# Performance work log

Measured on AMD Instinct MI355X. Metric: run time of the kernel, lower is better.

Reference implementation:

```python
import jax, jax.numpy as jnp
import numpy as np

EPS = 1e-12
H = 256
W = 256
RANK = 4
CTX = 1024
BATCH = 32
FF = (H + W) * RANK * 4  # 8192
STD = 0.001


def _norm(x, axis):
    # torch: (x - mean) / sqrt(var(unbiased) + eps)
    m = jnp.mean(x, axis=axis, keepdims=True)
    v = jnp.var(x, axis=axis, keepdims=True, ddof=1)
    return (x - m) / jnp.sqrt(v + EPS)


def _norm_polar(x):
    # x: [B, N, 2]; magnitude-normalize relative to per-batch max magnitude
    x_abs = jnp.sqrt(x[..., 0] ** 2 + x[..., 1] ** 2 + EPS)          # [B, N]
    h = x_abs / (jnp.max(x_abs, axis=-1, keepdims=True) + EPS)       # [B, N]
    xn = x / (x_abs[..., None] + EPS)                                # [B, N, 2]
    return jnp.stack([h * xn[..., 0], h * xn[..., 1]], axis=-1)


def setup_inputs() -> dict:
    key = jax.random.key(0)
    ks = jax.random.split(key, 12)

    def lin(k, fan_in, shape):
        b = 1.0 / np.sqrt(fan_in)
        return jax.random.uniform(k, shape, jnp.float32, -b, b)

    weights_static = jnp.concatenate([
        jax.random.normal(ks[9], (1, H, W, 2), jnp.float32) * STD,
        jax.random.normal(ks[10], (1, H, W, 2), jnp.float32) * STD
        + jnp.array([1.0, 0.0], jnp.float32),
    ], axis=0)  # [2, H, W, 2]

    return {
        "x": jax.random.normal(ks[0], (BATCH, CTX), jnp.float32),
        "W_in": lin(ks[1], CTX, (FF, CTX)),
        "b_in": lin(ks[2], CTX, (FF,)),
        "W_gate": lin(ks[3], CTX, (FF, CTX)),
        "b_gate": lin(ks[4], CTX, (FF,)),
        "W_t": lin(ks[5], FF, (FF, FF)),
        "b_t": lin(ks[6], FF, (FF,)),
        "conv_w": lin(ks[7], RANK, (RANK, RANK)),  # 1x1 conv kernel [out, in]
        "conv_b": lin(ks[8], RANK, (RANK,)),
        "weights_static": weights_static,
        "weights_mod": jax.random.normal(ks[11], (4, H, W), jnp.float32) * STD,
    }


def reference(x, W_in, b_in, W_gate, b_gate, W_t, b_t, conv_w, conv_b,
              weights_static, weights_mod):
    b = x.shape[0]
    # dual linear projections (dropout p=0 -> identity)
    xt = x @ W_in.T + b_in            # [B, FF]
    xg = x @ W_gate.T + b_gate        # [B, FF]
    stack = jnp.stack([xt, xg], axis=0).reshape(2, b, 4, -1)
    stack = _norm(stack, -1)
    ctx = (stack[0] * jnp.tanh(stack[1])).reshape(b, -1)   # gated, [B, FF]
    ctx = ctx @ W_t.T + b_t                                 # [B, FF]
    ctx = ctx.reshape(b, 4, RANK, H + W)
    modc = _norm(ctx, -1)
    # outer product -> [B, 4, RANK, H, W]
    mod = jnp.tanh(jnp.einsum('bkri,bkrj->bkrij', modc[..., :H], modc[..., H:]))
    # channel 0: 1x1 conv over rank channels, then sum channels (keepdim)
    mod_real = jnp.einsum('oi,bihw->bohw', conv_w, mod[:, 0]) + conv_b[None, :, None, None]
    mod_real = jnp.sum(mod_real, axis=1, keepdims=True)     # [B, 1, H, W]
    mod_other = jnp.sum(mod[:, 1:], axis=2)                 # [B, 3, H, W]
    mod = jnp.concatenate([mod_real, mod_other], axis=1)    # [B, 4, H, W]
    mod = weights_mod[None] * mod

    A0 = weights_static[0]            # [H, W, 2]
    A1 = weights_static[1]            # [H, W, 2]
    Bm = jnp.moveaxis(mod[:, 0:2], 1, -1)                   # [B, H, W, 2]
    ms_r = A1[..., 0] * Bm[..., 0] - A1[..., 1] * Bm[..., 1]
    ms_i = A1[..., 0] * Bm[..., 1] - A1[..., 1] * Bm[..., 0]
    mod_scaled = jnp.stack([ms_r, ms_i], axis=-1)           # [B, H, W, 2]
    mod_scaled = _norm_polar(mod_scaled.reshape(b, H * W, 2)).reshape(b, H, W, 2)

    mag = jnp.sqrt(mod_scaled[..., 0] ** 2 + mod_scaled[..., 1] ** 2 + EPS)
    mag = jnp.sqrt(jnp.mean(mag, axis=(-1, -2)) + EPS)      # [B]
    mod_scaled = mod_scaled / mag[:, None, None, None]

    mod_weights = A0[None] + mod_scaled                     # [B, H, W, 2]

    mod_proj = jnp.moveaxis(mod[:, 2:], 1, -1)              # [B, H, W, 2]
    mod_proj = _norm_polar(mod_proj.reshape(b, H * W, 2)).reshape(b, H, W, 2)
    den = jnp.sqrt(mod_proj[..., 0] ** 2 + mod_proj[..., 1] ** 2 + EPS)
    theta_cos = mod_proj[..., 0] / den
    theta_sin = mod_proj[..., 1] / den
    weights = mod_weights[..., 0] * theta_cos + mod_weights[..., 1] * theta_sin
    return weights  # [B, H, W]
```

## Files before the change

### kernel.cpp

```cpp
#include <hip/hip_runtime.h>
#include <cstddef>

#define NB   32
#define CTXD 1024
#define FFD  8192
#define HD   256
#define WD   256
#define NPIX 65536
#define EPSF 1e-12f

typedef __attribute__((ext_vector_type(8))) short bf16x8;
typedef __attribute__((ext_vector_type(4))) float f32x4;


__device__ __forceinline__ float ftanh(float x){
  float ax = fabsf(x);
  float e  = __expf(2.0f*ax);
  float r  = 1.0f - 2.0f*__builtin_amdgcn_rcpf(e + 1.0f);
  return copysignf(r, x);
}

__device__ __forceinline__ unsigned short f2bf(float f){
  unsigned u = __float_as_uint(f);
  unsigned r = (u + 0x7FFFu + ((u >> 16) & 1u)) >> 16;
  return (unsigned short)r;
}
__device__ __forceinline__ float bf2f(unsigned short s){
  return __uint_as_float((unsigned)s << 16);
}

__device__ __forceinline__ void split3(float f, unsigned short& s0,
                                       unsigned short& s1, unsigned short& s2){
  s0 = f2bf(f);
  float r1 = f - bf2f(s0);
  s1 = f2bf(r1);
  float r2 = r1 - bf2f(s1);
  s2 = f2bf(r2);
}

__device__ __forceinline__ void gload_lds16(const float* g, float* l){
  __builtin_amdgcn_global_load_lds(
      (__attribute__((address_space(1))) void*)const_cast<float*>(g),
      (__attribute__((address_space(3))) void*)l, 16, 0, 0);
}

__device__ __forceinline__ void block_reduce4(float& a, float& b, float& c, float& d){
  for (int off = 32; off > 0; off >>= 1){
    a += __shfl_down(a, off); b += __shfl_down(b, off);
    c += __shfl_down(c, off); d += __shfl_down(d, off);
  }
  __shared__ float lds[16];
  int wid = threadIdx.x >> 6, lane = threadIdx.x & 63;
  if (lane == 0){ lds[wid*4+0]=a; lds[wid*4+1]=b; lds[wid*4+2]=c; lds[wid*4+3]=d; }
  __syncthreads();
  a = (lds[0]+lds[4])+(lds[8]+lds[12]);
  b = (lds[1]+lds[5])+(lds[9]+lds[13]);
  c = (lds[2]+lds[6])+(lds[10]+lds[14]);
  d = (lds[3]+lds[7])+(lds[11]+lds[15]);
}

__device__ __forceinline__ void pixel_core(
    const float* __restrict__ lds, int h, int w, int pix,
    float cw0, float cw1, float cw2, float cw3, float cb,
    const float* __restrict__ wmod, const float* __restrict__ wstat,
    float& r_, float& i_, float& p_, float& q_){
  float sk[4];
  #pragma unroll
  for (int k = 0; k < 4; ++k){
    float acc = 0.f;
    #pragma unroll
    for (int r = 0; r < 4; ++r){
      int kr = k*4 + r;
      float u  = lds[kr*512 + h];
      float vv = lds[kr*512 + 256 + w];
      float tt = ftanh(u*vv);
      float cwr = (r==0)?cw0:(r==1)?cw1:(r==2)?cw2:cw3;
      acc += (k==0) ? cwr*tt : tt;
    }
    sk[k] = acc;
  }
  sk[0] += cb;
  float m0 = sk[0]*wmod[0*NPIX+pix];
  float m1 = sk[1]*wmod[1*NPIX+pix];
  float m2 = sk[2]*wmod[2*NPIX+pix];
  float m3 = sk[3]*wmod[3*NPIX+pix];
  float2 A1 = *(const float2*)(wstat + (size_t)(NPIX + pix)*2);
  r_ = A1.x*m0 - A1.y*m1;
  i_ = A1.x*m1 - A1.y*m0;
  p_ = m2; q_ = m3;
}


__global__ __launch_bounds__(256) void k_prep(
    const float* __restrict__ x, unsigned short* __restrict__ P,
    float* __restrict__ red){
  int g = blockIdx.x*256 + threadIdx.x;
  if (g < 64) red[g] = 0.0f;
  int b = g >> 7, grp = g & 127;
  int koff = grp*8;
  int c = grp >> 2, kg = grp & 3;
  const float* src = x + (size_t)b*CTXD + koff;
  float4 v0 = *(const float4*)(src), v1 = *(const float4*)(src+4);
  float vv[8] = {v0.x,v0.y,v0.z,v0.w,v1.x,v1.y,v1.z,v1.w};
  bf16x8 a0, a1, a2;
  #pragma unroll
  for (int e = 0; e < 8; ++e){
    unsigned short s0,s1,s2; split3(vv[e],s0,s1,s2);
    a0[e]=(short)s0; a1[e]=(short)s1; a2[e]=(short)s2;
  }
  size_t base = (size_t)c*3072 + (b>>4)*512 + kg*128 + (b&15)*8;
  *(bf16x8*)(P + base)        = a0;
  *(bf16x8*)(P + base + 1024) = a1;
  *(bf16x8*)(P + base + 2048) = a2;
}

template<int STEPS, int WROT>
__global__ __launch_bounds__(256) void k_gemm_lds(
    const float* __restrict__ W0, const float* __restrict__ W1,
    const unsigned short* __restrict__ BP,
    float* __restrict__ Cp, int K, size_t zstride){
  __shared__ float tile[2][4096];
  const int t    = threadIdx.x;
  const int wv   = t >> 6, lane = t & 63;
  const int f0   = blockIdx.x * 64;
  const int kc   = blockIdx.y;
  const int row  = lane & 15, kg = lane >> 4;
  const float* __restrict__ W = blockIdx.z ? W1 : W0;
  const int srot = ((int)blockIdx.x + wv*WROT) & (STEPS - 1);
  const size_t kslice = (size_t)kc * STEPS * 64;

  f32x4 acc0 = {0.f,0.f,0.f,0.f}, acc1 = {0.f,0.f,0.f,0.f};

  auto stage = [&](int buf, int sc){
    const size_t kbase = kslice + (size_t)sc*64;
    #pragma unroll
    for (int i = 0; i < 4; ++i){
      int r = wv*16 + i*4 + kg;
      const float* gsrc = W + (size_t)(f0 + r)*K + kbase + row*4;
      gload_lds16(gsrc, &tile[buf][(wv*16 + i*4)*64]);
    }
  };

  int cur = 0;
  stage(0, srot);
  for (int s = 0; s < STEPS; ++s){
    const int sc = (s + srot) & (STEPS - 1);
    const int k0 = kc*STEPS*2 + sc*2;
    const unsigned short* bp0 = BP + (size_t)k0*3072     + kg*128 + row*8;
    const unsigned short* bp1 = BP + (size_t)(k0+1)*3072 + kg*128 + row*8;
    bf16x8 c0b0h0 = *(const bf16x8*)(bp0);
    bf16x8 c0b0h1 = *(const bf16x8*)(bp0 +  512);
    bf16x8 c0b1h0 = *(const bf16x8*)(bp0 + 1024);
    bf16x8 c0b1h1 = *(const bf16x8*)(bp0 + 1536);
    bf16x8 c0b2h0 = *(const bf16x8*)(bp0 + 2048);
    bf16x8 c0b2h1 = *(const bf16x8*)(bp0 + 2560);
    bf16x8 c1b0h0 = *(const bf16x8*)(bp1);
    bf16x8 c1b0h1 = *(const bf16x8*)(bp1 +  512);
    bf16x8 c1b1h0 = *(const bf16x8*)(bp1 + 1024);
    bf16x8 c1b1h1 = *(const bf16x8*)(bp1 + 1536);
    bf16x8 c1b2h0 = *(const bf16x8*)(bp1 + 2048);
    bf16x8 c1b2h1 = *(const bf16x8*)(bp1 + 2560);
    if (s + 1 < STEPS) stage(cur ^ 1, (s + 1 + srot) & (STEPS - 1));
    asm volatile("s_waitcnt vmcnt(4)" ::: "memory");
    __builtin_amdgcn_sched_barrier(0);
    #pragma unroll
    for (int c = 0; c < 2; ++c){
      const float* wp = &tile[cur][(wv*16 + row)*64 + c*32 + kg*8];
      float4 w0 = *(const float4*)(wp);
      float4 w1 = *(const float4*)(wp + 4);
      bf16x8 a0, a1, a2;
      float wv8[8] = {w0.x,w0.y,w0.z,w0.w,w1.x,w1.y,w1.z,w1.w};
      #pragma unroll
      for (int e = 0; e < 8; ++e){
        unsigned short s0,s1,s2; split3(wv8[e],s0,s1,s2);
        a0[e]=(short)s0; a1[e]=(short)s1; a2[e]=(short)s2;
      }
      bf16x8 b0h0 = c ? c1b0h0 : c0b0h0, b0h1 = c ? c1b0h1 : c0b0h1;
      bf16x8 b1h0 = c ? c1b1h0 : c0b1h0, b1h1 = c ? c1b1h1 : c0b1h1;
      bf16x8 b2h0 = c ? c1b2h0 : c0b2h0, b2h1 = c ? c1b2h1 : c0b2h1;
      acc0 = __builtin_amdgcn_mfma_f32_16x16x32_bf16(a0, b0h0, acc0, 0,0,0);
      acc1 = __builtin_amdgcn_mfma_f32_16x16x32_bf16(a0, b0h1, acc1, 0,0,0);
      acc0 = __builtin_amdgcn_mfma_f32_16x16x32_bf16(a0, b1h0, acc0, 0,0,0);
      acc1 = __builtin_amdgcn_mfma_f32_16x16x32_bf16(a0, b1h1, acc1, 0,0,0);
      acc0 = __builtin_amdgcn_mfma_f32_16x16x32_bf16(a1, b0h0, acc0, 0,0,0);
      acc1 = __builtin_amdgcn_mfma_f32_16x16x32_bf16(a1, b0h1, acc1, 0,0,0);
      acc0 = __builtin_amdgcn_mfma_f32_16x16x32_bf16(a0, b2h0, acc0, 0,0,0);
      acc1 = __builtin_amdgcn_mfma_f32_16x16x32_bf16(a0, b2h1, acc1, 0,0,0);
      acc0 = __builtin_amdgcn_mfma_f32_16x16x32_bf16(a1, b1h0, acc0, 0,0,0);
      acc1 = __builtin_amdgcn_mfma_f32_16x16x32_bf16(a1, b1h1, acc1, 0,0,0);
      acc0 = __builtin_amdgcn_mfma_f32_16x16x32_bf16(a2, b0h0, acc0, 0,0,0);
      acc1 = __builtin_amdgcn_mfma_f32_16x16x32_bf16(a2, b0h1, acc1, 0,0,0);
    }
    cur ^= 1;
  }

  float* __restrict__ C = Cp + (size_t)blockIdx.z*zstride + (size_t)kc*(FFD*32);
  #pragma unroll
  for (int r = 0; r < 4; ++r){
    int f = f0 + wv*16 + kg*4 + r;
    C[(size_t)f*32 + row]      = acc0[r];
    C[(size_t)f*32 + 16 + row] = acc1[r];
  }
}

__global__ __launch_bounds__(256) void k_reduce1(
    const float* __restrict__ Cp, const float* __restrict__ bin,
    const float* __restrict__ bg, float* __restrict__ xtT,
    float* __restrict__ xgT){
  int g = blockIdx.x*256 + threadIdx.x;
  int m = g >> 18, idx = g & 262143;
  int f = idx >> 5;
  const float* __restrict__ cp = Cp + (size_t)m*(4ull*FFD*32);
  float s = (m ? bg : bin)[f];
  #pragma unroll
  for (int sI = 0; sI < 4; ++sI) s += cp[(size_t)sI*(FFD*32) + idx];
  (m ? xgT : xtT)[idx] = s;
}

__global__ __launch_bounds__(256) void k_reduce2(
    const float* __restrict__ Cp, const float* __restrict__ bias,
    float* __restrict__ outT){
  int g = blockIdx.x*256 + threadIdx.x;
  int f = g >> 5;
  float s = bias[f];
  #pragma unroll
  for (int sI = 0; sI < 16; ++sI) s += Cp[(size_t)sI*(FFD*32) + g];
  outT[g] = s;
}

__global__ __launch_bounds__(256) void k_normgate(
    const float* __restrict__ xtT, const float* __restrict__ xgT,
    unsigned short* __restrict__ P){
  int b = blockIdx.x >> 2, g4 = blockIdx.x & 3;
  int t = threadIdx.x;
  int f8 = g4*2048 + t*8;
  float vt[8], vg[8];
  float st=0.f, sst=0.f, sg=0.f, ssg=0.f;
  #pragma unroll
  for (int i = 0; i < 8; ++i){
    int f = f8 + i;
    float a = xtT[(size_t)f*NB + b];
    float c = xgT[(size_t)f*NB + b];
    vt[i]=a; vg[i]=c;
    st += a; sst += a*a; sg += c; ssg += c*c;
  }
  block_reduce4(st, sst, sg, ssg);
  float mt = st * (1.0f/2048.0f);
  float it = rsqrtf((sst - st*mt) * (1.0f/2047.0f) + EPSF);
  float mg = sg * (1.0f/2048.0f);
  float ig = rsqrtf((ssg - sg*mg) * (1.0f/2047.0f) + EPSF);
  bf16x8 a0, a1, a2;
  #pragma unroll
  for (int i = 0; i < 8; ++i){
    float nt = (vt[i]-mt)*it;
    float ng = (vg[i]-mg)*ig;
    float cv = nt * ftanh(ng);
    unsigned short s0,s1,s2; split3(cv,s0,s1,s2);
    a0[i]=(short)s0; a1[i]=(short)s1; a2[i]=(short)s2;
  }
  int c2 = f8 >> 5, kg = (f8 >> 3) & 3;
  size_t base = (size_t)c2*3072 + (b>>4)*512 + kg*128 + (b&15)*8;
  *(bf16x8*)(P + base)        = a0;
  *(bf16x8*)(P + base + 1024) = a1;
  *(bf16x8*)(P + base + 2048) = a2;
}

__global__ __launch_bounds__(256) void k_norm512(
    const float* __restrict__ ctx2T, float* __restrict__ modc){
  int b = blockIdx.x >> 4, kr = blockIdx.x & 15;
  int t = threadIdx.x;
  int base = kr*512;
  float v0 = ctx2T[(base + t      )*NB + b];
  float v1 = ctx2T[(base + 256 + t)*NB + b];
  float s = v0+v1, ss = v0*v0 + v1*v1, d0=0.f, d1=0.f;
  block_reduce4(s, ss, d0, d1);
  float m   = s * (1.0f/512.0f);
  float inv = rsqrtf((ss - s*m) * (1.0f/511.0f) + EPSF);
  modc[b*FFD + base + t      ] = (v0-m)*inv;
  modc[b*FFD + base + 256 + t] = (v1-m)*inv;
}

__global__ __launch_bounds__(256) void k_scan(
    const float* __restrict__ modc,
    const float* __restrict__ convw, const float* __restrict__ convb,
    const float* __restrict__ wmod, const float* __restrict__ wstat,
    float* __restrict__ red, float* __restrict__ magpart){
  int b = blockIdx.x >> 4, chunk = blockIdx.x & 15;
  int t = threadIdx.x;
  __shared__ float lds[16*512];
  #pragma unroll
  for (int i = 0; i < 8; ++i){
    float4 v = *(const float4*)(modc + (size_t)b*FFD + (i*256 + t)*4);
    *(float4*)(lds + (i*256 + t)*4) = v;
  }
  float cw0 = convw[0]+convw[4]+convw[8]+convw[12];
  float cw1 = convw[1]+convw[5]+convw[9]+convw[13];
  float cw2 = convw[2]+convw[6]+convw[10]+convw[14];
  float cw3 = convw[3]+convw[7]+convw[11]+convw[15];
  float cb  = convb[0]+convb[1]+convb[2]+convb[3];
  __syncthreads();
  int w = t;
  float mxs = 0.f, mxp = 0.f, sas = 0.f;
  for (int it = 0; it < 16; ++it){
    int h = chunk*16 + it;
    int pix = h*WD + w;
    float r_, i_, p_, q_;
    pixel_core(lds, h, w, pix, cw0, cw1, cw2, cw3, cb, wmod, wstat,
               r_, i_, p_, q_);
    float as = sqrtf(r_*r_ + i_*i_ + EPSF);
    float ap = sqrtf(p_*p_ + q_*q_ + EPSF);
    mxs = fmaxf(mxs, as); mxp = fmaxf(mxp, ap);
    sas += as;
  }
  for (int off = 32; off > 0; off >>= 1){
    mxs = fmaxf(mxs, __shfl_down(mxs, off));
    mxp = fmaxf(mxp, __shfl_down(mxp, off));
    sas += __shfl_down(sas, off);
  }
  __shared__ float lred[12];
  int wid = t >> 6, lane = t & 63;
  if (lane == 0){ lred[wid] = mxs; lred[4+wid] = mxp; lred[8+wid] = sas; }
  __syncthreads();
  if (t == 0){
    float a = fmaxf(fmaxf(lred[0],lred[1]), fmaxf(lred[2],lred[3]));
    float p = fmaxf(fmaxf(lred[4],lred[5]), fmaxf(lred[6],lred[7]));
    float s = (lred[8]+lred[9])+(lred[10]+lred[11]);
    atomicMax((int*)&red[b],    __float_as_int(a));
    atomicMax((int*)&red[32+b], __float_as_int(p));
    magpart[b*16 + chunk] = s;
  }
}

__global__ __launch_bounds__(256) void k_final(
    const float* __restrict__ modc,
    const float* __restrict__ convw, const float* __restrict__ convb,
    const float* __restrict__ wmod, const float* __restrict__ wstat,
    const float* __restrict__ red, const float* __restrict__ magpart,
    float* __restrict__ out){
  int b = blockIdx.x >> 4, chunk = blockIdx.x & 15;
  int t = threadIdx.x;
  __shared__ float lds[16*512];
  __shared__ float s_im;
  if (t < 16){
    float v = magpart[b*16 + t];
    for (int off = 8; off > 0; off >>= 1) v += __shfl_down(v, off);
    if (t == 0){
      float maxs = red[b];
      s_im = rsqrtf(v*(1.0f/65536.0f)/(maxs + EPSF) + EPSF);
    }
  }
  #pragma unroll
  for (int i = 0; i < 8; ++i){
    float4 v = *(const float4*)(modc + (size_t)b*FFD + (i*256 + t)*4);
    *(float4*)(lds + (i*256 + t)*4) = v;
  }
  float cw0 = convw[0]+convw[4]+convw[8]+convw[12];
  float cw1 = convw[1]+convw[5]+convw[9]+convw[13];
  float cw2 = convw[2]+convw[6]+convw[10]+convw[14];
  float cw3 = convw[3]+convw[7]+convw[11]+convw[15];
  float cb  = convb[0]+convb[1]+convb[2]+convb[3];
  __syncthreads();
  float im = s_im;
  float maxs = red[b], maxp = red[32+b];
  int w = t;
  for (int it = 0; it < 16; ++it){
    int h = chunk*16 + it;
    int pix = h*WD + w;
    float r_, i_, p_, q_;
    pixel_core(lds, h, w, pix, cw0, cw1, cw2, cw3, cb, wmod, wstat,
               r_, i_, p_, q_);
    float as = sqrtf(r_*r_ + i_*i_ + EPSF);
    float fs = (as/(maxs+EPSF))/(as+EPSF)*im;
    float2 A0 = *(const float2*)(wstat + (size_t)pix*2);
    float mwr = A0.x + fs*r_;
    float mwi = A0.y + fs*i_;
    float ap = sqrtf(p_*p_ + q_*q_ + EPSF);
    float fp = (ap/(maxp+EPSF))/(ap+EPSF);
    float mpr = fp*p_, mpi = fp*q_;
    float den = sqrtf(mpr*mpr + mpi*mpi + EPSF);
    out[(size_t)b*NPIX + pix] = (mwr*mpr + mwi*mpi)/den;
  }
}


extern "C" void kernel_launch(void* const* d_in, const int* in_sizes, int n_in,
                              void* d_out, int out_size, void* d_ws, size_t ws_size,
                              hipStream_t stream){
  const float* x     = (const float*)d_in[0];
  const float* Win   = (const float*)d_in[1];
  const float* bin   = (const float*)d_in[2];
  const float* Wg    = (const float*)d_in[3];
  const float* bg    = (const float*)d_in[4];
  const float* Wt    = (const float*)d_in[5];
  const float* bt    = (const float*)d_in[6];
  const float* convw = (const float*)d_in[7];
  const float* convb = (const float*)d_in[8];
  const float* wstat = (const float*)d_in[9];
  const float* wmod  = (const float*)d_in[10];
  float* out = (float*)d_out;
  float* ws  = (float*)d_ws;

  float* xtT   = ws;
  float* xgT   = ws + 262144;
  float* ctx2T = ws;
  float* modc  = ws + 262144;
  unsigned short* P2 = (unsigned short*)(ws + 524288);
  unsigned short* P1 = (unsigned short*)(ws + 917504);
  float* Cp    = ws + 966656;
  float* red     = ws + 5160960;
  float* magpart = ws + 5161024;

  k_prep<<<16, 256, 0, stream>>>(x, P1, red);
  k_gemm_lds<4,1><<<dim3(128,4,2), 256, 0, stream>>>(Win, Wg, P1,
                                                     Cp, CTXD, 4ull*FFD*32);
  k_reduce1<<<2048, 256, 0, stream>>>(Cp, bin, bg, xtT, xgT);
  k_normgate<<<128, 256, 0, stream>>>(xtT, xgT, P2);
  k_gemm_lds<8,2><<<dim3(128,16,1), 256, 0, stream>>>(Wt, Wt, P2,
                                                      Cp, FFD, 0);
  k_reduce2<<<1024, 256, 0, stream>>>(Cp, bt, ctx2T);
  k_norm512<<<512, 256, 0, stream>>>(ctx2T, modc);
  k_scan<<<512, 256, 0, stream>>>(modc, convw, convb, wmod, wstat, red, magpart);
  k_final<<<512, 256, 0, stream>>>(modc, convw, convb, wmod, wstat, red,
                                   magpart, out);
}
```

Measured before the change: 163.9 us.

## Replace double-buffered GEMM with single-shot streaming kernel and finer split-K

```diff
diff --git a/kernel.cpp b/kernel.cpp
--- a/kernel.cpp
+++ b/kernel.cpp
@@ -114,90 +114,79 @@
   *(bf16x8*)(P + base + 2048) = a2;
 }
 
-template<int STEPS, int WROT>
-__global__ __launch_bounds__(256) void k_gemm_lds(
+__global__ __launch_bounds__(128) void k_gemm_stream(
     const float* __restrict__ W0, const float* __restrict__ W1,
     const unsigned short* __restrict__ BP,
     float* __restrict__ Cp, int K, size_t zstride){
-  __shared__ float tile[2][4096];
+  __shared__ float tile[8192];
   const int t    = threadIdx.x;
   const int wv   = t >> 6, lane = t & 63;
-  const int f0   = blockIdx.x * 64;
+  const int row  = lane & 15, kg = lane >> 4;
+  const int f0   = blockIdx.x*32 + wv*16;
   const int kc   = blockIdx.y;
-  const int row  = lane & 15, kg = lane >> 4;
   const float* __restrict__ W = blockIdx.z ? W1 : W0;
-  const int srot = ((int)blockIdx.x + wv*WROT) & (STEPS - 1);
-  const size_t kslice = (size_t)kc * STEPS * 64;
+  const int kb   = kc*256;
+
+  float* ldst = tile + wv*4096;
+  const float* wbase = W + (size_t)f0*K + kb;
+  #pragma unroll
+  for (int r = 0; r < 16; ++r){
+    const float* src = wbase + (size_t)r*K + ((lane ^ (r & 7)) << 2);
+    gload_lds16(src, ldst + r*256);
+  }
+  const unsigned short* pb = BP + (size_t)(kc*8)*3072 + kg*128 + row*8;
+  bf16x8 b0 = *(const bf16x8*)(pb);
+  bf16x8 b1 = *(const bf16x8*)(pb +  512);
+  bf16x8 b2 = *(const bf16x8*)(pb + 1024);
+  bf16x8 b3 = *(const bf16x8*)(pb + 1536);
+  bf16x8 b4 = *(const bf16x8*)(pb + 2048);
+  bf16x8 b5 = *(const bf16x8*)(pb + 2560);
+  asm volatile("s_waitcnt vmcnt(0)" ::: "memory");
+  __builtin_amdgcn_sched_barrier(0);
 
   f32x4 acc0 = {0.f,0.f,0.f,0.f}, acc1 = {0.f,0.f,0.f,0.f};
-
-  auto stage = [&](int buf, int sc){
-    const size_t kbase = kslice + (size_t)sc*64;
+  const float* lrow = tile + wv*4096 + row*256;
+  const int sw = row & 7;
+  #pragma unroll
+  for (int c = 0; c < 8; ++c){
+    bf16x8 cb0=b0, cb1=b1, cb2=b2, cb3=b3, cb4=b4, cb5=b5;
+    if (c < 7){
+      const unsigned short* pn = pb + (size_t)(c+1)*3072;
+      b0 = *(const bf16x8*)(pn);
+      b1 = *(const bf16x8*)(pn +  512);
+      b2 = *(const bf16x8*)(pn + 1024);
+      b3 = *(const bf16x8*)(pn + 1536);
+      b4 = *(const bf16x8*)(pn + 2048);
+      b5 = *(const bf16x8*)(pn + 2560);
+    }
+    int q = c*8 + kg*2;
+    float4 lo = *(const float4*)(lrow + ((q      ^ sw) << 2));
+    float4 hi = *(const float4*)(lrow + (((q+1) ^ sw) << 2));
+    bf16x8 a0, a1, a2;
+    float wv8[8] = {lo.x,lo.y,lo.z,lo.w,hi.x,hi.y,hi.z,hi.w};
     #pragma unroll
-    for (int i = 0; i < 4; ++i){
-      int r = wv*16 + i*4 + kg;
-      const float* gsrc = W + (size_t)(f0 + r)*K + kbase + row*4;
-      gload_lds16(gsrc, &tile[buf][(wv*16 + i*4)*64]);
+    for (int e = 0; e < 8; ++e){
+      unsigned short s0,s1,s2; split3(wv8[e],s0,s1,s2);
+      a0[e]=(short)s0; a1[e]=(short)s1; a2[e]=(short)s2;
     }
-  };
-
-  int cur = 0;
-  stage(0, srot);
-  for (int s = 0; s < STEPS; ++s){
-    const int sc = (s + srot) & (STEPS - 1);
-    const int k0 = kc*STEPS*2 + sc*2;
-    const unsigned short* bp0 = BP + (size_t)k0*3072     + kg*128 + row*8;
-    const unsigned short* bp1 = BP + (size_t)(k0+1)*3072 + kg*128 + row*8;
-    bf16x8 c0b0h0 = *(const bf16x8*)(bp0);
-    bf16x8 c0b0h1 = *(const bf16x8*)(bp0 +  512);
-    bf16x8 c0b1h0 = *(const bf16x8*)(bp0 + 1024);
-    bf16x8 c0b1h1 = *(const bf16x8*)(bp0 + 1536);
-    bf16x8 c0b2h0 = *(const bf16x8*)(bp0 + 2048);
-    bf16x8 c0b2h1 = *(const bf16x8*)(bp0 + 2560);
-    bf16x8 c1b0h0 = *(const bf16x8*)(bp1);
-    bf16x8 c1b0h1 = *(const bf16x8*)(bp1 +  512);
-    bf16x8 c1b1h0 = *(const bf16x8*)(bp1 + 1024);
-    bf16x8 c1b1h1 = *(const bf16x8*)(bp1 + 1536);
-    bf16x8 c1b2h0 = *(const bf16x8*)(bp1 + 2048);
-    bf16x8 c1b2h1 = *(const bf16x8*)(bp1 + 2560);
-    if (s + 1 < STEPS) stage(cur ^ 1, (s + 1 + srot) & (STEPS - 1));
-    asm volatile("s_waitcnt vmcnt(4)" ::: "memory");
-    __builtin_amdgcn_sched_barrier(0);
-    #pragma unroll
-    for (int c = 0; c < 2; ++c){
-      const float* wp = &tile[cur][(wv*16 + row)*64 + c*32 + kg*8];
-      float4 w0 = *(const float4*)(wp);
-      float4 w1 = *(const float4*)(wp + 4);
-      bf16x8 a0, a1, a2;
-      float wv8[8] = {w0.x,w0.y,w0.z,w0.w,w1.x,w1.y,w1.z,w1.w};
-      #pragma unroll
-      for (int e = 0; e < 8; ++e){
-        unsigned short s0,s1,s2; split3(wv8[e],s0,s1,s2);
-        a0[e]=(short)s0; a1[e]=(short)s1; a2[e]=(short)s2;
-      }
-      bf16x8 b0h0 = c ? c1b0h0 : c0b0h0, b0h1 = c ? c1b0h1 : c0b0h1;
-      bf16x8 b1h0 = c ? c1b1h0 : c0b1h0, b1h1 = c ? c1b1h1 : c0b1h1;
-      bf16x8 b2h0 = c ? c1b2h0 : c0b2h0, b2h1 = c ? c1b2h1 : c0b2h1;
-      acc0 = __builtin_amdgcn_mfma_f32_16x16x32_bf16(a0, b0h0, acc0, 0,0,0);
-      acc1 = __builtin_amdgcn_mfma_f32_16x16x32_bf16(a0, b0h1, acc1, 0,0,0);
-      acc0 = __builtin_amdgcn_mfma_f32_16x16x32_bf16(a0, b1h0, acc0, 0,0,0);
-      acc1 = __builtin_amdgcn_mfma_f32_16x16x32_bf16(a0, b1h1, acc1, 0,0,0);
-      acc0 = __builtin_amdgcn_mfma_f32_16x16x32_bf16(a1, b0h0, acc0, 0,0,0);
-      acc1 = __builtin_amdgcn_mfma_f32_16x16x32_bf16(a1, b0h1, acc1, 0,0,0);
-      acc0 = __builtin_amdgcn_mfma_f32_16x16x32_bf16(a0, b2h0, acc0, 0,0,0);
-      acc1 = __builtin_amdgcn_mfma_f32_16x16x32_bf16(a0, b2h1, acc1, 0,0,0);
-      acc0 = __builtin_amdgcn_mfma_f32_16x16x32_bf16(a1, b1h0, acc0, 0,0,0);
-      acc1 = __builtin_amdgcn_mfma_f32_16x16x32_bf16(a1, b1h1, acc1, 0,0,0);
-      acc0 = __builtin_amdgcn_mfma_f32_16x16x32_bf16(a2, b0h0, acc0, 0,0,0);
-      acc1 = __builtin_amdgcn_mfma_f32_16x16x32_bf16(a2, b0h1, acc1, 0,0,0);
-    }
-    cur ^= 1;
+    acc0 = __builtin_amdgcn_mfma_f32_16x16x32_bf16(a0, cb0, acc0, 0,0,0);
+    acc1 = __builtin_amdgcn_mfma_f32_16x16x32_bf16(a0, cb1, acc1, 0,0,0);
+    acc0 = __builtin_amdgcn_mfma_f32_16x16x32_bf16(a0, cb2, acc0, 0,0,0);
+    acc1 = __builtin_amdgcn_mfma_f32_16x16x32_bf16(a0, cb3, acc1, 0,0,0);
+    acc0 = __builtin_amdgcn_mfma_f32_16x16x32_bf16(a1, cb0, acc0, 0,0,0);
+    acc1 = __builtin_amdgcn_mfma_f32_16x16x32_bf16(a1, cb1, acc1, 0,0,0);
+    acc0 = __builtin_amdgcn_mfma_f32_16x16x32_bf16(a0, cb4, acc0, 0,0,0);
+    acc1 = __builtin_amdgcn_mfma_f32_16x16x32_bf16(a0, cb5, acc1, 0,0,0);
+    acc0 = __builtin_amdgcn_mfma_f32_16x16x32_bf16(a1, cb2, acc0, 0,0,0);
+    acc1 = __builtin_amdgcn_mfma_f32_16x16x32_bf16(a1, cb3, acc1, 0,0,0);
+    acc0 = __builtin_amdgcn_mfma_f32_16x16x32_bf16(a2, cb0, acc0, 0,0,0);
+    acc1 = __builtin_amdgcn_mfma_f32_16x16x32_bf16(a2, cb1, acc1, 0,0,0);
   }
 
   float* __restrict__ C = Cp + (size_t)blockIdx.z*zstride + (size_t)kc*(FFD*32);
   #pragma unroll
   for (int r = 0; r < 4; ++r){
-    int f = f0 + wv*16 + kg*4 + r;
+    int f = f0 + kg*4 + r;
     C[(size_t)f*32 + row]      = acc0[r];
     C[(size_t)f*32 + 16 + row] = acc1[r];
   }
@@ -224,7 +213,7 @@
   int f = g >> 5;
   float s = bias[f];
   #pragma unroll
-  for (int sI = 0; sI < 16; ++sI) s += Cp[(size_t)sI*(FFD*32) + g];
+  for (int sI = 0; sI < 32; ++sI) s += Cp[(size_t)sI*(FFD*32) + g];
   outT[g] = s;
 }
 
@@ -407,16 +396,16 @@
   unsigned short* P2 = (unsigned short*)(ws + 524288);
   unsigned short* P1 = (unsigned short*)(ws + 917504);
   float* Cp    = ws + 966656;
-  float* red     = ws + 5160960;
-  float* magpart = ws + 5161024;
+  float* red     = ws + 9355264;
+  float* magpart = ws + 9355328;
 
   k_prep<<<16, 256, 0, stream>>>(x, P1, red);
-  k_gemm_lds<4,1><<<dim3(128,4,2), 256, 0, stream>>>(Win, Wg, P1,
-                                                     Cp, CTXD, 4ull*FFD*32);
+  k_gemm_stream<<<dim3(256,4,2), 128, 0, stream>>>(Win, Wg, P1,
+                                                   Cp, CTXD, 4ull*FFD*32);
   k_reduce1<<<2048, 256, 0, stream>>>(Cp, bin, bg, xtT, xgT);
   k_normgate<<<128, 256, 0, stream>>>(xtT, xgT, P2);
-  k_gemm_lds<8,2><<<dim3(128,16,1), 256, 0, stream>>>(Wt, Wt, P2,
-                                                      Cp, FFD, 0);
+  k_gemm_stream<<<dim3(256,32,1), 128, 0, stream>>>(Wt, Wt, P2,
+                                                    Cp, FFD, 0);
   k_reduce2<<<1024, 256, 0, stream>>>(Cp, bt, ctx2T);
   k_norm512<<<512, 256, 0, stream>>>(ctx2T, modc);
   k_scan<<<512, 256, 0, stream>>>(modc, convw, convb, wmod, wstat, red, magpart);
```

Result: slower. 173.6 us (+6.0%).
